# Performance work log

Measured on AMD Instinct MI355X. Metric: run time of the kernel, lower is better.

Reference implementation:

```python
import jax, jax.numpy as jnp
import numpy as np

EMBED_DIM = 1024
NUM_HEADS = 16
HEAD_DIM = EMBED_DIM // NUM_HEADS
EXPANSION = 4
EPS = 1e-5


def setup_inputs() -> dict:
    key = jax.random.key(0)
    ks = jax.random.split(key, 8)
    D, F = EMBED_DIM, EMBED_DIM * EXPANSION
    s = lambda d: 1.0 / np.sqrt(d)
    return {
        "x": jax.random.normal(ks[0], (8, 1024, D), jnp.float32),
        "qkv_w": jax.random.normal(ks[1], (D, 3 * D), jnp.float32) * s(D),
        "qkv_b": jnp.zeros((3 * D,), jnp.float32),
        "out_w": jax.random.normal(ks[2], (D, D), jnp.float32) * s(D),
        "out_b": jnp.zeros((D,), jnp.float32),
        "ffn_w1": jax.random.normal(ks[3], (D, F), jnp.float32) * s(D),
        "ffn_b1": jnp.zeros((F,), jnp.float32),
        "ffn_w2": jax.random.normal(ks[4], (F, D), jnp.float32) * s(F),
        "ffn_b2": jnp.zeros((D,), jnp.float32),
        "ln1_g": jnp.ones((D,), jnp.float32),
        "ln1_b": jnp.zeros((D,), jnp.float32),
        "ln2_g": jnp.ones((D,), jnp.float32),
        "ln2_b": jnp.zeros((D,), jnp.float32),
    }


def _layernorm(x, g, b):
    mu = jnp.mean(x, axis=-1, keepdims=True)
    var = jnp.mean(jnp.square(x - mu), axis=-1, keepdims=True)
    return (x - mu) * jax.lax.rsqrt(var + EPS) * g + b


def reference(x, qkv_w, qkv_b, out_w, out_b, ffn_w1, ffn_b1, ffn_w2, ffn_b2,
              ln1_g, ln1_b, ln2_g, ln2_b):
    B, N, D = x.shape
    H, Hd = NUM_HEADS, HEAD_DIM
    scale = Hd ** -0.5

    residual = x
    h = _layernorm(x, ln1_g, ln1_b)
    qkv = h @ qkv_w + qkv_b                      # [B, N, 3D]
    q, k, v = jnp.split(qkv, 3, axis=-1)
    # [B, N, D] -> [B, H, N, Hd]
    reshape = lambda t: t.reshape(B, N, H, Hd).transpose(0, 2, 1, 3)
    q, k, v = reshape(q), reshape(k), reshape(v)

    attn = jnp.einsum("bhnd,bhmd->bhnm", q, k) * scale
    attn = jax.nn.softmax(attn, axis=-1)
    o = jnp.einsum("bhnm,bhmd->bhnd", attn, v)   # [B, H, N, Hd]
    o = o.transpose(0, 2, 1, 3).reshape(B, N, D)
    o = o @ out_w + out_b
    x = residual + o

    residual = x
    h = _layernorm(x, ln2_g, ln2_b)
    h = jax.nn.gelu(h @ ffn_w1 + ffn_b1, approximate=False) @ ffn_w2 + ffn_b2
    return residual + h
```

## Files before the change

kernel.cpp:

```cpp
#include <hip/hip_runtime.h>
#include <hip/hip_bf16.h>


typedef float f32x4 __attribute__((ext_vector_type(4)));
typedef float f32x16 __attribute__((ext_vector_type(16)));
typedef short bf16x8 __attribute__((ext_vector_type(8)));

#define DEV __device__ __forceinline__

DEV f32x4 mfma16(bf16x8 a, bf16x8 b, f32x4 c) {
    return __builtin_amdgcn_mfma_f32_16x16x32_bf16(a, b, c, 0, 0, 0);
}

DEV f32x16 mfma32(bf16x8 a, bf16x8 b, f32x16 c) {
    return __builtin_amdgcn_mfma_f32_32x32x16_bf16(a, b, c, 0, 0, 0);
}

DEV ushort f2bf(float f) {
    union { float f; unsigned u; } v; v.f = f;
    unsigned r = v.u + 0x7FFFu + ((v.u >> 16) & 1u);
    return (ushort)(r >> 16);
}

DEV unsigned cvtpk(float lo, float hi) {
    unsigned r;
    asm("v_cvt_pk_bf16_f32 %0, %1, %2" : "=v"(r) : "v"(lo), "v"(hi));
    return r;
}

DEV void gload_lds16(const void* g, void* l) {
    __builtin_amdgcn_global_load_lds(
        (const __attribute__((address_space(1))) void*)g,
        (__attribute__((address_space(3))) void*)l, 16, 0, 0);
}

template <int N> DEV void vmwait() {
    asm volatile("s_waitcnt vmcnt(%0)" :: "n"(N) : "memory");
}
DEV void lgkm0() {
    asm volatile("s_waitcnt lgkmcnt(0)" ::: "memory");
}

__global__ __launch_bounds__(256) void transpose_w(
    const float* __restrict__ src, ushort* __restrict__ dst, int K, int N)
{
    __shared__ float tile[32][33];
    const int n0 = blockIdx.x * 32, k0 = blockIdx.y * 32;
    const int tx = threadIdx.x, ty = threadIdx.y;
#pragma unroll
    for (int i = 0; i < 32; i += 8)
        tile[ty + i][tx] = src[(size_t)(k0 + ty + i) * N + n0 + tx];
    __syncthreads();
#pragma unroll
    for (int i = 0; i < 32; i += 8)
        dst[(size_t)(n0 + ty + i) * K + k0 + tx] = f2bf(tile[tx][ty + i]);
}

__global__ __launch_bounds__(256) void transpose_v(
    const ushort* __restrict__ qkvb, ushort* __restrict__ vt)
{
    __shared__ ushort tile[32][33];
    const int b = blockIdx.z >> 4, h = blockIdx.z & 15;
    const int n0 = blockIdx.x * 32, d0 = blockIdx.y * 32;
    const int tx = threadIdx.x, ty = threadIdx.y;
#pragma unroll
    for (int i = 0; i < 32; i += 8)
        tile[ty + i][tx] =
            qkvb[(size_t)(b * 1024 + n0 + ty + i) * 3072 + 2048 + h * 64 + d0 + tx];
    __syncthreads();
#pragma unroll
    for (int i = 0; i < 32; i += 8)
        vt[((size_t)(b * 16 + h) * 64 + d0 + ty + i) * 1024 + n0 + tx] = tile[tx][ty + i];
}

__global__ __launch_bounds__(256) void ln_bf16(
    const float* __restrict__ x, const float* __restrict__ gw,
    const float* __restrict__ bw, ushort* __restrict__ out)
{
    const int row = blockIdx.x;
    const int t = threadIdx.x;
    const float4 v = ((const float4*)(x + (size_t)row * 1024))[t];
    float s  = v.x + v.y + v.z + v.w;
    float s2 = v.x * v.x + v.y * v.y + v.z * v.z + v.w * v.w;
#pragma unroll
    for (int off = 32; off; off >>= 1) {
        s  += __shfl_xor(s, off);
        s2 += __shfl_xor(s2, off);
    }
    __shared__ float red[16];
    const int wave = t >> 6, lane = t & 63;
    if (lane == 0) { red[wave] = s; red[8 + wave] = s2; }
    __syncthreads();
    s  = red[0] + red[1] + red[2] + red[3];
    s2 = red[8] + red[9] + red[10] + red[11];
    const float mean = s * (1.0f / 1024.0f);
    const float var  = s2 * (1.0f / 1024.0f) - mean * mean;
    const float rstd = rsqrtf(var + 1e-5f);
    const float4 gv = ((const float4*)gw)[t];
    const float4 bv = ((const float4*)bw)[t];
    ushort4 o;
    o.x = f2bf((v.x - mean) * rstd * gv.x + bv.x);
    o.y = f2bf((v.y - mean) * rstd * gv.y + bv.y);
    o.z = f2bf((v.z - mean) * rstd * gv.z + bv.z);
    o.w = f2bf((v.w - mean) * rstd * gv.w + bv.w);
    ((ushort4*)out)[(size_t)row * 256 + t] = o;
}

template <int BM, int BN, int WM_, int WN_, int EPI>
__global__ __launch_bounds__(512, 2) void gemm4p(
    const ushort* __restrict__ A, const ushort* __restrict__ BT,
    const float* __restrict__ bias, const float* __restrict__ res,
    void* __restrict__ out, int M, int N, int K)
{
    constexpr int BK = 64;
    constexpr int MR = BM / WM_ / 16;
    constexpr int NR = BN / WN_ / 16;
    constexpr int MH = MR / 2;
    constexpr int CM = MH / 2;
    constexpr int LA = (BM / 2) / 64;
    constexpr int LB = (BN / 2) / 64;
    constexpr int VMN = LA + LB;
    constexpr int ABYTES = BM * BK * 2;
    constexpr int BBYTES = BN * BK * 2;

    extern __shared__ __align__(16) char smem[];
#define ASB(b) (smem + (b) * ABYTES)
#define BSB(b) (smem + 2 * ABYTES + (b) * BBYTES)

    const int tid = threadIdx.x;
    const int wave = tid >> 6, lane = tid & 63;
    const int g = lane >> 4, lr = lane & 15;
    const int wr = wave / WN_, wc = wave % WN_;
    const int akey = (lr & 7) << 4;

    const int gx = gridDim.x;
    const int nwg = gx * gridDim.y;
    int id = blockIdx.y * gx + blockIdx.x;
    id = (id & 7) * (nwg >> 3) + (id >> 3);
    const int m0 = (id / gx) * BM, n0 = (id % gx) * BN;

    const int trow = tid >> 3;
    const int tblk = (tid & 7) ^ (trow & 7);
    const ushort* pA = A  + (size_t)(m0 + trow) * K + tblk * 8;
    const ushort* pB = BT + (size_t)(n0 + trow) * K + tblk * 8;
    const int woff = wave * 1024;

#define STAGE_A(b, h, kt) do { \
    _Pragma("unroll") for (int i = 0; i < LA; ++i) \
        gload_lds16(pA + ((size_t)((h) * (BM / 2) + i * 64)) * K + (size_t)(kt) * 64, \
                    ASB(b) + (h) * (BM / 2) * 128 + i * 8192 + woff); \
} while (0)
#define STAGE_B(b, h, kt) do { \
    _Pragma("unroll") for (int i = 0; i < LB; ++i) \
        gload_lds16(pB + ((size_t)((h) * (BN / 2) + i * 64)) * K + (size_t)(kt) * 64, \
                    BSB(b) + (h) * (BN / 2) * 128 + i * 8192 + woff); \
} while (0)

    bf16x8 af[CM][2], bfr[NR][2];
    f32x4 acc[MR][NR] = {};

#define LOAD_A(b, h, cj) do { \
    const char* rb_ = ASB(b) + ((h) * (BM / 2) + wr * ((BM / 2) / WM_) \
                               + (cj) * CM * 16 + lr) * 128; \
    _Pragma("unroll") for (int cm = 0; cm < CM; ++cm) \
    _Pragma("unroll") for (int kk = 0; kk < 2; ++kk) \
        af[cm][kk] = *(const bf16x8*)(rb_ + cm * 2048 + ((kk * 64 + g * 16) ^ akey)); \
} while (0)
#define LOAD_B(b) do { \
    const char* rb_ = BSB(b) + (wc * (BN / WN_) + lr) * 128; \
    _Pragma("unroll") for (int ni = 0; ni < NR; ++ni) \
    _Pragma("unroll") for (int kk = 0; kk < 2; ++kk) \
        bfr[ni][kk] = *(const bf16x8*)(rb_ + ni * 2048 + ((kk * 64 + g * 16) ^ akey)); \
} while (0)
#define MFMA_PH(h, cj) do { \
    __builtin_amdgcn_s_setprio(1); \
    _Pragma("unroll") for (int cm = 0; cm < CM; ++cm) \
    _Pragma("unroll") for (int ni = 0; ni < NR; ++ni) \
    _Pragma("unroll") for (int kk = 0; kk < 2; ++kk) \
        acc[(h) * MH + (cj) * CM + cm][ni] = \
            mfma16(af[cm][kk], bfr[ni][kk], acc[(h) * MH + (cj) * CM + cm][ni]); \
    __builtin_amdgcn_s_setprio(0); \
} while (0)

    const int NT = K >> 6;

    STAGE_A(0, 0, 0); STAGE_A(0, 1, 0); STAGE_B(0, 0, 0); STAGE_B(0, 1, 0);
    STAGE_B(1, 0, 1);
    STAGE_A(1, 0, 1);
    vmwait<VMN>();
    __builtin_amdgcn_s_barrier();

    for (int kt = 0; kt < NT; ++kt) {
        const int b = kt & 1, nb = b ^ 1;
        LOAD_A(b, 0, 0); LOAD_B(b);
        if (kt + 1 < NT) STAGE_B(nb, 1, kt + 1);
        __builtin_amdgcn_s_barrier(); lgkm0();
        MFMA_PH(0, 0);
        LOAD_A(b, 0, 1);
        if (kt + 1 < NT) STAGE_A(nb, 1, kt + 1);
        __builtin_amdgcn_s_barrier(); lgkm0();
        MFMA_PH(0, 1);
        LOAD_A(b, 1, 0);
        if (kt + 2 < NT) STAGE_B(b, 0, kt + 2);
        __builtin_amdgcn_s_barrier(); lgkm0();
        MFMA_PH(1, 0);
        LOAD_A(b, 1, 1);
        if (kt + 2 < NT) { STAGE_A(b, 0, kt + 2); vmwait<VMN>(); }
        else if (kt + 1 < NT) vmwait<0>();
        __builtin_amdgcn_s_barrier(); lgkm0();
        MFMA_PH(1, 1);
    }

#pragma unroll
    for (int mi = 0; mi < MR; ++mi) {
        const int row0 = m0 + (mi / MH) * (BM / 2) + wr * ((BM / 2) / WM_)
                       + (mi % MH) * 16 + 4 * g;
#pragma unroll
        for (int ni = 0; ni < NR; ++ni) {
            const int col = n0 + wc * (BN / WN_) + ni * 16 + lr;
            const float bv = bias[col];
#pragma unroll
            for (int r = 0; r < 4; ++r) {
                float v = acc[mi][ni][r] + bv;
                const size_t idx = (size_t)(row0 + r) * N + col;
                if constexpr (EPI == 1) {
                    ((float*)out)[idx] = v + res[idx];
                } else if constexpr (EPI == 2) {
                    const float u = 1.595769122f * v + 0.071354816f * v * v * v;
                    const float gs = 1.0f / (1.0f + __expf(-u));
                    ((ushort*)out)[idx] = f2bf(v * gs);
                } else {
                    ((ushort*)out)[idx] = f2bf(v);
                }
            }
        }
    }
#undef STAGE_A
#undef STAGE_B
#undef LOAD_A
#undef LOAD_B
#undef MFMA_PH
#undef ASB
#undef BSB
}

__global__ __launch_bounds__(256) void attn_kernel(
    const ushort* __restrict__ qkv, const ushort* __restrict__ vtb,
    ushort* __restrict__ o)
{
    __shared__ __align__(16) ushort Ks[64 * 64];
    __shared__ __align__(16) ushort Vt[64 * 64];

    const int tid = threadIdx.x;
    const int wave = tid >> 6, lane = tid & 63;
    const int lq = lane & 31;
    const int hi = lane >> 5;
    const int l7 = lane & 7;

    const int hwid = blockIdx.x;
    const int logical = (hwid & 7) * 128 + (hwid >> 3);
    const int bh = logical >> 3, qt = logical & 7;
    const int b = bh >> 4, head = bh & 15;
    const int q0 = qt * 128 + wave * 32;

    const size_t base  = (size_t)b * 1024 * 3072;
    const size_t vbase = (size_t)bh * 64 * 1024;

    union BF8 { bf16x8 v; ushort u[8]; unsigned w[4]; };

    BF8 qf[4];
    {
        const ushort* qrow = qkv + base + (size_t)(q0 + lq) * 3072 + head * 64;
#pragma unroll
        for (int s = 0; s < 4; ++s) {
            *(ushort4*)&qf[s].u[0] = *(const ushort4*)(qrow + 16 * s + 4 * hi);
            *(ushort4*)&qf[s].u[4] = *(const ushort4*)(qrow + 16 * s + 8 + 4 * hi);
        }
    }

    const int sr = tid >> 3, sc = tid & 7;
    const int swz = (sc ^ (sr & 7)) << 3;
    const ushort* kg0 = qkv + base + (size_t)sr * 3072 + 1024 + head * 64 + sc * 8;
    const ushort* kg1 = kg0 + (size_t)32 * 3072;
    const ushort* vg0 = vtb + vbase + (size_t)sr * 1024 + sc * 8;
    const ushort* vg1 = vg0 + (size_t)32 * 1024;
    ushort* ksw0 = Ks + sr * 64 + swz;
    ushort* ksw1 = Ks + (sr + 32) * 64 + swz;
    ushort* vsw0 = Vt + sr * 64 + swz;
    ushort* vsw1 = Vt + (sr + 32) * 64 + swz;

    float l_st = 0.f;
    f32x16 oacc[2] = {};

    constexpr float SCL = 0.18033688011112042f;
    constexpr float MBIAS = 12.0f;

    for (int kt = 0; kt < 16; ++kt) {
        const int n0 = kt * 64;
        __syncthreads();
        *(bf16x8*)ksw0 = *(const bf16x8*)(kg0 + (size_t)n0 * 3072);
        *(bf16x8*)ksw1 = *(const bf16x8*)(kg1 + (size_t)n0 * 3072);
        *(bf16x8*)vsw0 = *(const bf16x8*)(vg0 + n0);
        *(bf16x8*)vsw1 = *(const bf16x8*)(vg1 + n0);
        __syncthreads();

        f32x16 sacc[2];
#pragma unroll
        for (int kb = 0; kb < 2; ++kb) {
            f32x16 a = {};
            const ushort* krow = Ks + (kb * 32 + lq) * 64;
#pragma unroll
            for (int s = 0; s < 4; ++s) {
                BF8 kf;
                *(ushort4*)&kf.u[0] = *(const ushort4*)(krow + (((2 * s)     ^ l7) << 3) + 4 * hi);
                *(ushort4*)&kf.u[4] = *(const ushort4*)(krow + (((2 * s + 1) ^ l7) << 3) + 4 * hi);
                a = mfma32(kf.v, qf[s].v, a);
            }
            sacc[kb] = a;
        }

        float p0 = 0.f, p1 = 0.f, p2 = 0.f, p3 = 0.f;
#pragma unroll
        for (int kb = 0; kb < 2; ++kb)
#pragma unroll
            for (int r = 0; r < 16; ++r) {
                const float pe = exp2f(fmaf(sacc[kb][r], SCL, -MBIAS));
                sacc[kb][r] = pe;
                if ((r & 3) == 0)      p0 += pe;
                else if ((r & 3) == 1) p1 += pe;
                else if ((r & 3) == 2) p2 += pe;
                else                   p3 += pe;
            }
        float psum = (p0 + p1) + (p2 + p3);
        psum += __shfl_xor(psum, 32);
        l_st += psum;

#pragma unroll
        for (int kb = 0; kb < 2; ++kb) {
            BF8 pf[2];
#pragma unroll
            for (int t = 0; t < 2; ++t)
#pragma unroll
                for (int w = 0; w < 4; ++w)
                    pf[t].w[w] = cvtpk(sacc[kb][8 * t + 2 * w], sacc[kb][8 * t + 2 * w + 1]);
#pragma unroll
            for (int nb = 0; nb < 2; ++nb) {
                const ushort* vrow = Vt + (nb * 32 + lq) * 64;
#pragma unroll
                for (int t = 0; t < 2; ++t) {
                    BF8 vf;
                    const int blk = 4 * kb + 2 * t;
                    *(ushort4*)&vf.u[0] = *(const ushort4*)(vrow + ((blk       ^ l7) << 3) + 4 * hi);
                    *(ushort4*)&vf.u[4] = *(const ushort4*)(vrow + (((blk + 1) ^ l7) << 3) + 4 * hi);
                    oacc[nb] = mfma32(vf.v, pf[t].v, oacc[nb]);
                }
            }
        }
    }

    const float inv = 1.0f / l_st;
    ushort* orow = o + (size_t)(b * 1024 + q0 + lq) * 1024 + head * 64;
#pragma unroll
    for (int nb = 0; nb < 2; ++nb)
#pragma unroll
        for (int u = 0; u < 4; ++u) {
            uint2 wv;
            wv.x = cvtpk(oacc[nb][4 * u] * inv,     oacc[nb][4 * u + 1] * inv);
            wv.y = cvtpk(oacc[nb][4 * u + 2] * inv, oacc[nb][4 * u + 3] * inv);
            *(uint2*)(orow + nb * 32 + 8 * u + 4 * hi) = wv;
        }
}

extern "C" void kernel_launch(void* const* d_in, const int* in_sizes, int n_in,
                              void* d_out, int out_size, void* d_ws, size_t ws_size,
                              hipStream_t stream)
{
    const float* x      = (const float*)d_in[0];
    const float* qkv_w  = (const float*)d_in[1];
    const float* qkv_b  = (const float*)d_in[2];
    const float* out_w  = (const float*)d_in[3];
    const float* out_b  = (const float*)d_in[4];
    const float* ffn_w1 = (const float*)d_in[5];
    const float* ffn_b1 = (const float*)d_in[6];
    const float* ffn_w2 = (const float*)d_in[7];
    const float* ffn_b2 = (const float*)d_in[8];
    const float* ln1_g  = (const float*)d_in[9];
    const float* ln1_b  = (const float*)d_in[10];
    const float* ln2_g  = (const float*)d_in[11];
    const float* ln2_b  = (const float*)d_in[12];

    constexpr size_t MB = 1u << 20;
    char* ws = (char*)d_ws;
    ushort* wt_qkv = (ushort*)(ws + 0 * MB);
    ushort* wt_out = (ushort*)(ws + 6 * MB);
    ushort* wt_f1  = (ushort*)(ws + 8 * MB);
    ushort* wt_f2  = (ushort*)(ws + 16 * MB);
    float*  x1     = (float*) (ws + 24 * MB);
    ushort* vtb    = (ushort*)(ws + 24 * MB);
    ushort* hbuf   = (ushort*)(ws + 56 * MB);
    ushort* qkvb   = (ushort*)(ws + 72 * MB);
    ushort* obuf   = (ushort*)(ws + 120 * MB);
    ushort* gbuf   = (ushort*)(ws + 72 * MB);

    const dim3 tb(32, 8);
    transpose_w<<<dim3(3072 / 32, 1024 / 32), tb, 0, stream>>>(qkv_w,  wt_qkv, 1024, 3072);
    transpose_w<<<dim3(1024 / 32, 1024 / 32), tb, 0, stream>>>(out_w,  wt_out, 1024, 1024);
    transpose_w<<<dim3(4096 / 32, 1024 / 32), tb, 0, stream>>>(ffn_w1, wt_f1,  1024, 4096);
    transpose_w<<<dim3(1024 / 32, 4096 / 32), tb, 0, stream>>>(ffn_w2, wt_f2,  4096, 1024);

    ln_bf16<<<8192, 256, 0, stream>>>(x, ln1_g, ln1_b, hbuf);

    constexpr int LDS_256 = (256 + 256) * 64 * 2 * 2;
    constexpr int LDS_128 = (256 + 128) * 64 * 2 * 2;

    gemm4p<256, 256, 2, 4, 0><<<dim3(12, 32), 512, LDS_256, stream>>>(
        hbuf, wt_qkv, qkv_b, nullptr, qkvb, 8192, 3072, 1024);

    transpose_v<<<dim3(32, 2, 128), tb, 0, stream>>>(qkvb, vtb);

    attn_kernel<<<1024, 256, 0, stream>>>(qkvb, vtb, obuf);

    gemm4p<256, 128, 4, 2, 1><<<dim3(8, 32), 512, LDS_128, stream>>>(
        obuf, wt_out, out_b, x, x1, 8192, 1024, 1024);

    ln_bf16<<<8192, 256, 0, stream>>>(x1, ln2_g, ln2_b, hbuf);

    gemm4p<256, 256, 2, 4, 2><<<dim3(16, 32), 512, LDS_256, stream>>>(
        hbuf, wt_f1, ffn_b1, nullptr, gbuf, 8192, 4096, 1024);

    gemm4p<256, 128, 4, 2, 1><<<dim3(8, 32), 512, LDS_128, stream>>>(
        gbuf, wt_f2, ffn_b2, x1, (float*)d_out, 8192, 1024, 4096);
}
```

Measured before the change: 344.9 us.

## Replace templated GEMM with triple-buffered register-prefetch 256x128 GEMM for all projections

Replaces the double-buffered, barrier-per-quarter gemm4p with a fixed 256x128 tile GEMM that uses three LDS buffers. It double-buffers A/B fragments in registers so LDS reads for the next half overlap the current MFMAs. The QKV and FFN1 GEMMs move from 256x256 tiles to 256x128, which doubles their grid size. The aim is to hide global-to-LDS and LDS-to-register latency behind MFMA work, at the cost of more LDS per block (144 KB), possible lower occupancy, and more A-tile re-reads on the wide GEMMs.

```diff
diff --git a/kernel.cpp b/kernel.cpp
--- a/kernel.cpp
+++ b/kernel.cpp
@@ -106,31 +106,22 @@
     ((ushort4*)out)[(size_t)row * 256 + t] = o;
 }
 
-template <int BM, int BN, int WM_, int WN_, int EPI>
-__global__ __launch_bounds__(512, 2) void gemm4p(
+template <int EPI>
+__global__ __launch_bounds__(512, 2) void gemm_ra(
     const ushort* __restrict__ A, const ushort* __restrict__ BT,
     const float* __restrict__ bias, const float* __restrict__ res,
     void* __restrict__ out, int M, int N, int K)
 {
-    constexpr int BK = 64;
-    constexpr int MR = BM / WM_ / 16;
-    constexpr int NR = BN / WN_ / 16;
-    constexpr int MH = MR / 2;
-    constexpr int CM = MH / 2;
-    constexpr int LA = (BM / 2) / 64;
-    constexpr int LB = (BN / 2) / 64;
-    constexpr int VMN = LA + LB;
+    constexpr int BM = 256, BN = 128, BK = 64;
     constexpr int ABYTES = BM * BK * 2;
-    constexpr int BBYTES = BN * BK * 2;
+    constexpr int BUF = ABYTES + BN * BK * 2;
 
     extern __shared__ __align__(16) char smem[];
-#define ASB(b) (smem + (b) * ABYTES)
-#define BSB(b) (smem + 2 * ABYTES + (b) * BBYTES)
 
     const int tid = threadIdx.x;
     const int wave = tid >> 6, lane = tid & 63;
     const int g = lane >> 4, lr = lane & 15;
-    const int wr = wave / WN_, wc = wave % WN_;
+    const int wr = wave >> 1, wc = wave & 1;
     const int akey = (lr & 7) << 4;
 
     const int gx = gridDim.x;
@@ -145,79 +136,89 @@
     const ushort* pB = BT + (size_t)(n0 + trow) * K + tblk * 8;
     const int woff = wave * 1024;
 
-#define STAGE_A(b, h, kt) do { \
-    _Pragma("unroll") for (int i = 0; i < LA; ++i) \
-        gload_lds16(pA + ((size_t)((h) * (BM / 2) + i * 64)) * K + (size_t)(kt) * 64, \
-                    ASB(b) + (h) * (BM / 2) * 128 + i * 8192 + woff); \
+#define STAGE_A(dst, kt) do { \
+    _Pragma("unroll") for (int i = 0; i < 4; ++i) \
+        gload_lds16(pA + (size_t)(i * 64) * K + (size_t)(kt) * 64, \
+                    (dst) + i * 8192 + woff); \
 } while (0)
-#define STAGE_B(b, h, kt) do { \
-    _Pragma("unroll") for (int i = 0; i < LB; ++i) \
-        gload_lds16(pB + ((size_t)((h) * (BN / 2) + i * 64)) * K + (size_t)(kt) * 64, \
-                    BSB(b) + (h) * (BN / 2) * 128 + i * 8192 + woff); \
+#define STAGE_B(dst, kt) do { \
+    _Pragma("unroll") for (int i = 0; i < 2; ++i) \
+        gload_lds16(pB + (size_t)(i * 64) * K + (size_t)(kt) * 64, \
+                    (dst) + ABYTES + i * 8192 + woff); \
 } while (0)
 
-    bf16x8 af[CM][2], bfr[NR][2];
-    f32x4 acc[MR][NR] = {};
-
-#define LOAD_A(b, h, cj) do { \
-    const char* rb_ = ASB(b) + ((h) * (BM / 2) + wr * ((BM / 2) / WM_) \
-                               + (cj) * CM * 16 + lr) * 128; \
-    _Pragma("unroll") for (int cm = 0; cm < CM; ++cm) \
+    bf16x8 aX[2][2], aY[2][2], bP[4][2], bQ[4][2];
+    f32x4 acc[4][4] = {};
+
+#define READ_A(SET, buf, h) do { \
+    const char* rb_ = (buf) + (wr * 64 + (h) * 32 + lr) * 128; \
+    _Pragma("unroll") for (int mi = 0; mi < 2; ++mi) \
     _Pragma("unroll") for (int kk = 0; kk < 2; ++kk) \
-        af[cm][kk] = *(const bf16x8*)(rb_ + cm * 2048 + ((kk * 64 + g * 16) ^ akey)); \
+        SET[mi][kk] = *(const bf16x8*)(rb_ + mi * 2048 + ((kk * 64 + g * 16) ^ akey)); \
 } while (0)
-#define LOAD_B(b) do { \
-    const char* rb_ = BSB(b) + (wc * (BN / WN_) + lr) * 128; \
-    _Pragma("unroll") for (int ni = 0; ni < NR; ++ni) \
+#define READ_B(SET, buf) do { \
+    const char* rb_ = (buf) + ABYTES + (wc * 64 + lr) * 128; \
+    _Pragma("unroll") for (int ni = 0; ni < 4; ++ni) \
     _Pragma("unroll") for (int kk = 0; kk < 2; ++kk) \
-        bfr[ni][kk] = *(const bf16x8*)(rb_ + ni * 2048 + ((kk * 64 + g * 16) ^ akey)); \
+        SET[ni][kk] = *(const bf16x8*)(rb_ + ni * 2048 + ((kk * 64 + g * 16) ^ akey)); \
 } while (0)
-#define MFMA_PH(h, cj) do { \
+#define MFMA_H(ASET, h, BSET) do { \
     __builtin_amdgcn_s_setprio(1); \
-    _Pragma("unroll") for (int cm = 0; cm < CM; ++cm) \
-    _Pragma("unroll") for (int ni = 0; ni < NR; ++ni) \
     _Pragma("unroll") for (int kk = 0; kk < 2; ++kk) \
-        acc[(h) * MH + (cj) * CM + cm][ni] = \
-            mfma16(af[cm][kk], bfr[ni][kk], acc[(h) * MH + (cj) * CM + cm][ni]); \
+    _Pragma("unroll") for (int mi = 0; mi < 2; ++mi) \
+    _Pragma("unroll") for (int ni = 0; ni < 4; ++ni) \
+        acc[(h) * 2 + mi][ni] = \
+            mfma16(ASET[mi][kk], BSET[ni][kk], acc[(h) * 2 + mi][ni]); \
     __builtin_amdgcn_s_setprio(0); \
 } while (0)
+#define BAR() __builtin_amdgcn_s_barrier()
 
     const int NT = K >> 6;
 
-    STAGE_A(0, 0, 0); STAGE_A(0, 1, 0); STAGE_B(0, 0, 0); STAGE_B(0, 1, 0);
-    STAGE_B(1, 0, 1);
-    STAGE_A(1, 0, 1);
-    vmwait<VMN>();
-    __builtin_amdgcn_s_barrier();
-
-    for (int kt = 0; kt < NT; ++kt) {
-        const int b = kt & 1, nb = b ^ 1;
-        LOAD_A(b, 0, 0); LOAD_B(b);
-        if (kt + 1 < NT) STAGE_B(nb, 1, kt + 1);
-        __builtin_amdgcn_s_barrier(); lgkm0();
-        MFMA_PH(0, 0);
-        LOAD_A(b, 0, 1);
-        if (kt + 1 < NT) STAGE_A(nb, 1, kt + 1);
-        __builtin_amdgcn_s_barrier(); lgkm0();
-        MFMA_PH(0, 1);
-        LOAD_A(b, 1, 0);
-        if (kt + 2 < NT) STAGE_B(b, 0, kt + 2);
-        __builtin_amdgcn_s_barrier(); lgkm0();
-        MFMA_PH(1, 0);
-        LOAD_A(b, 1, 1);
-        if (kt + 2 < NT) { STAGE_A(b, 0, kt + 2); vmwait<VMN>(); }
-        else if (kt + 1 < NT) vmwait<0>();
-        __builtin_amdgcn_s_barrier(); lgkm0();
-        MFMA_PH(1, 1);
+    char* pb0 = smem;
+    char* pb1 = smem + BUF;
+    char* pb2 = smem + 2 * BUF;
+
+    STAGE_A(pb0, 0); STAGE_B(pb0, 0);
+    STAGE_A(pb1, 1); STAGE_B(pb1, 1);
+    vmwait<6>();
+    BAR();
+    READ_A(aX, pb0, 0);
+    READ_B(bP, pb0);
+
+    for (int t = 0; t < NT; t += 2) {
+        lgkm0();
+        READ_A(aY, pb0, 1);
+        if (t + 2 < NT) STAGE_A(pb2, t + 2);
+        MFMA_H(aX, 0, bP);
+        if (t + 2 < NT) vmwait<4>(); else vmwait<0>();
+        BAR();
+        lgkm0();
+        READ_A(aX, pb1, 0);
+        READ_B(bQ, pb1);
+        if (t + 2 < NT) STAGE_B(pb2, t + 2);
+        MFMA_H(aY, 1, bP);
+        BAR();
+        lgkm0();
+        READ_A(aY, pb1, 1);
+        if (t + 3 < NT) STAGE_A(pb0, t + 3);
+        MFMA_H(aX, 0, bQ);
+        if (t + 3 < NT) vmwait<4>(); else vmwait<0>();
+        BAR();
+        lgkm0();
+        if (t + 2 < NT) { READ_A(aX, pb2, 0); READ_B(bP, pb2); }
+        if (t + 3 < NT) STAGE_B(pb0, t + 3);
+        MFMA_H(aY, 1, bQ);
+        BAR();
+        char* tmp = pb0; pb0 = pb2; pb2 = pb1; pb1 = tmp;
     }
 
 #pragma unroll
-    for (int mi = 0; mi < MR; ++mi) {
-        const int row0 = m0 + (mi / MH) * (BM / 2) + wr * ((BM / 2) / WM_)
-                       + (mi % MH) * 16 + 4 * g;
-#pragma unroll
-        for (int ni = 0; ni < NR; ++ni) {
-            const int col = n0 + wc * (BN / WN_) + ni * 16 + lr;
+    for (int mi = 0; mi < 4; ++mi) {
+        const int row0 = m0 + wr * 64 + mi * 16 + 4 * g;
+#pragma unroll
+        for (int ni = 0; ni < 4; ++ni) {
+            const int col = n0 + wc * 64 + ni * 16 + lr;
             const float bv = bias[col];
 #pragma unroll
             for (int r = 0; r < 4; ++r) {
@@ -237,11 +238,10 @@
     }
 #undef STAGE_A
 #undef STAGE_B
-#undef LOAD_A
-#undef LOAD_B
-#undef MFMA_PH
-#undef ASB
-#undef BSB
+#undef READ_A
+#undef READ_B
+#undef MFMA_H
+#undef BAR
 }
 
 __global__ __launch_bounds__(256) void attn_kernel(
@@ -410,24 +410,23 @@
 
     ln_bf16<<<8192, 256, 0, stream>>>(x, ln1_g, ln1_b, hbuf);
 
-    constexpr int LDS_256 = (256 + 256) * 64 * 2 * 2;
-    constexpr int LDS_128 = (256 + 128) * 64 * 2 * 2;
-
-    gemm4p<256, 256, 2, 4, 0><<<dim3(12, 32), 512, LDS_256, stream>>>(
+    constexpr int LDS_RA = 3 * (256 * 64 * 2 + 128 * 64 * 2);
+
+    gemm_ra<0><<<dim3(24, 32), 512, LDS_RA, stream>>>(
         hbuf, wt_qkv, qkv_b, nullptr, qkvb, 8192, 3072, 1024);
 
     transpose_v<<<dim3(32, 2, 128), tb, 0, stream>>>(qkvb, vtb);
 
     attn_kernel<<<1024, 256, 0, stream>>>(qkvb, vtb, obuf);
 
-    gemm4p<256, 128, 4, 2, 1><<<dim3(8, 32), 512, LDS_128, stream>>>(
+    gemm_ra<1><<<dim3(8, 32), 512, LDS_RA, stream>>>(
         obuf, wt_out, out_b, x, x1, 8192, 1024, 1024);
 
     ln_bf16<<<8192, 256, 0, stream>>>(x1, ln2_g, ln2_b, hbuf);
 
-    gemm4p<256, 256, 2, 4, 2><<<dim3(16, 32), 512, LDS_256, stream>>>(
+    gemm_ra<2><<<dim3(32, 32), 512, LDS_RA, stream>>>(
         hbuf, wt_f1, ffn_b1, nullptr, gbuf, 8192, 4096, 1024);
 
-    gemm4p<256, 128, 4, 2, 1><<<dim3(8, 32), 512, LDS_128, stream>>>(
+    gemm_ra<1><<<dim3(8, 32), 512, LDS_RA, stream>>>(
         gbuf, wt_f2, ffn_b2, x1, (float*)d_out, 8192, 1024, 4096);
 }
```

Result: slower. 353.4 us (+2.5%).

## Store mid-block residual in bf16, fold attention scale into QKV GEMM, retile QKV

Applied to the files above, without the earlier changes.

The attention-output GEMM now writes the intermediate residual x1 as bf16 instead of fp32. A new bf16-input LayerNorm kernel and a new FFN2 epilogue (EPI 3) read that bf16 residual, which cuts memory traffic on the intermediate. The softmax scale (including log2e) is applied to the Q columns in the QKV GEMM epilogue, and the constant exp bias is removed, so the attention inner loop calls exp2 directly on the scores. The QKV GEMM switches from 256x256 to 256x128 tiles with twice as many blocks. The trade-offs are reduced precision on the residual path and no overflow guard in the softmax exponent.

```diff
diff --git a/kernel.cpp b/kernel.cpp
--- a/kernel.cpp
+++ b/kernel.cpp
@@ -22,6 +22,11 @@
     return (ushort)(r >> 16);
 }
 
+DEV float bf2f(ushort u) {
+    union { unsigned u; float f; } v; v.u = (unsigned)u << 16;
+    return v.f;
+}
+
 DEV unsigned cvtpk(float lo, float hi) {
     unsigned r;
     asm("v_cvt_pk_bf16_f32 %0, %1, %2" : "=v"(r) : "v"(lo), "v"(hi));
@@ -40,6 +45,8 @@
 DEV void lgkm0() {
     asm volatile("s_waitcnt lgkmcnt(0)" ::: "memory");
 }
+
+constexpr float ATT_SCL = 0.18033688011112042f;
 
 __global__ __launch_bounds__(256) void transpose_w(
     const float* __restrict__ src, ushort* __restrict__ dst, int K, int N)
@@ -106,6 +113,40 @@
     ((ushort4*)out)[(size_t)row * 256 + t] = o;
 }
 
+__global__ __launch_bounds__(256) void ln_bf16b(
+    const ushort* __restrict__ x, const float* __restrict__ gw,
+    const float* __restrict__ bw, ushort* __restrict__ out)
+{
+    const int row = blockIdx.x;
+    const int t = threadIdx.x;
+    const ushort4 uv = ((const ushort4*)(x + (size_t)row * 1024))[t];
+    float vx = bf2f(uv.x), vy = bf2f(uv.y), vz = bf2f(uv.z), vw = bf2f(uv.w);
+    float s  = vx + vy + vz + vw;
+    float s2 = vx * vx + vy * vy + vz * vz + vw * vw;
+#pragma unroll
+    for (int off = 32; off; off >>= 1) {
+        s  += __shfl_xor(s, off);
+        s2 += __shfl_xor(s2, off);
+    }
+    __shared__ float red[16];
+    const int wave = t >> 6, lane = t & 63;
+    if (lane == 0) { red[wave] = s; red[8 + wave] = s2; }
+    __syncthreads();
+    s  = red[0] + red[1] + red[2] + red[3];
+    s2 = red[8] + red[9] + red[10] + red[11];
+    const float mean = s * (1.0f / 1024.0f);
+    const float var  = s2 * (1.0f / 1024.0f) - mean * mean;
+    const float rstd = rsqrtf(var + 1e-5f);
+    const float4 gv = ((const float4*)gw)[t];
+    const float4 bv = ((const float4*)bw)[t];
+    ushort4 o;
+    o.x = f2bf((vx - mean) * rstd * gv.x + bv.x);
+    o.y = f2bf((vy - mean) * rstd * gv.y + bv.y);
+    o.z = f2bf((vz - mean) * rstd * gv.z + bv.z);
+    o.w = f2bf((vw - mean) * rstd * gv.w + bv.w);
+    ((ushort4*)out)[(size_t)row * 256 + t] = o;
+}
+
 template <int BM, int BN, int WM_, int WN_, int EPI>
 __global__ __launch_bounds__(512, 2) void gemm4p(
     const ushort* __restrict__ A, const ushort* __restrict__ BT,
@@ -116,7 +157,7 @@
     constexpr int MR = BM / WM_ / 16;
     constexpr int NR = BN / WN_ / 16;
     constexpr int MH = MR / 2;
-    constexpr int CM = MH / 2;
+    constexpr int CM = MH / 2 > 0 ? MH / 2 : 1;
     constexpr int LA = (BM / 2) / 64;
     constexpr int LB = (BN / 2) / 64;
     constexpr int VMN = LA + LB;
@@ -224,12 +265,15 @@
                 float v = acc[mi][ni][r] + bv;
                 const size_t idx = (size_t)(row0 + r) * N + col;
                 if constexpr (EPI == 1) {
-                    ((float*)out)[idx] = v + res[idx];
+                    ((ushort*)out)[idx] = f2bf(v + res[idx]);
                 } else if constexpr (EPI == 2) {
                     const float u = 1.595769122f * v + 0.071354816f * v * v * v;
                     const float gs = 1.0f / (1.0f + __expf(-u));
                     ((ushort*)out)[idx] = f2bf(v * gs);
+                } else if constexpr (EPI == 3) {
+                    ((float*)out)[idx] = v + bf2f(((const ushort*)res)[idx]);
                 } else {
+                    if (col < 1024) v *= ATT_SCL;
                     ((ushort*)out)[idx] = f2bf(v);
                 }
             }
@@ -292,9 +336,6 @@
     float l_st = 0.f;
     f32x16 oacc[2] = {};
 
-    constexpr float SCL = 0.18033688011112042f;
-    constexpr float MBIAS = 12.0f;
-
     for (int kt = 0; kt < 16; ++kt) {
         const int n0 = kt * 64;
         __syncthreads();
@@ -324,7 +365,7 @@
         for (int kb = 0; kb < 2; ++kb)
 #pragma unroll
             for (int r = 0; r < 16; ++r) {
-                const float pe = exp2f(fmaf(sacc[kb][r], SCL, -MBIAS));
+                const float pe = exp2f(sacc[kb][r]);
                 sacc[kb][r] = pe;
                 if ((r & 3) == 0)      p0 += pe;
                 else if ((r & 3) == 1) p1 += pe;
@@ -395,8 +436,8 @@
     ushort* wt_out = (ushort*)(ws + 6 * MB);
     ushort* wt_f1  = (ushort*)(ws + 8 * MB);
     ushort* wt_f2  = (ushort*)(ws + 16 * MB);
-    float*  x1     = (float*) (ws + 24 * MB);
-    ushort* vtb    = (ushort*)(ws + 24 * MB);
+    ushort* x1b    = (ushort*)(ws + 24 * MB);
+    ushort* vtb    = (ushort*)(ws + 40 * MB);
     ushort* hbuf   = (ushort*)(ws + 56 * MB);
     ushort* qkvb   = (ushort*)(ws + 72 * MB);
     ushort* obuf   = (ushort*)(ws + 120 * MB);
@@ -413,7 +454,7 @@
     constexpr int LDS_256 = (256 + 256) * 64 * 2 * 2;
     constexpr int LDS_128 = (256 + 128) * 64 * 2 * 2;
 
-    gemm4p<256, 256, 2, 4, 0><<<dim3(12, 32), 512, LDS_256, stream>>>(
+    gemm4p<256, 128, 4, 2, 4><<<dim3(24, 32), 512, LDS_128, stream>>>(
         hbuf, wt_qkv, qkv_b, nullptr, qkvb, 8192, 3072, 1024);
 
     transpose_v<<<dim3(32, 2, 128), tb, 0, stream>>>(qkvb, vtb);
@@ -421,13 +462,13 @@
     attn_kernel<<<1024, 256, 0, stream>>>(qkvb, vtb, obuf);
 
     gemm4p<256, 128, 4, 2, 1><<<dim3(8, 32), 512, LDS_128, stream>>>(
-        obuf, wt_out, out_b, x, x1, 8192, 1024, 1024);
-
-    ln_bf16<<<8192, 256, 0, stream>>>(x1, ln2_g, ln2_b, hbuf);
+        obuf, wt_out, out_b, x, x1b, 8192, 1024, 1024);
+
+    ln_bf16b<<<8192, 256, 0, stream>>>(x1b, ln2_g, ln2_b, hbuf);
 
     gemm4p<256, 256, 2, 4, 2><<<dim3(16, 32), 512, LDS_256, stream>>>(
         hbuf, wt_f1, ffn_b1, nullptr, gbuf, 8192, 4096, 1024);
 
-    gemm4p<256, 128, 4, 2, 1><<<dim3(8, 32), 512, LDS_128, stream>>>(
-        gbuf, wt_f2, ffn_b2, x1, (float*)d_out, 8192, 1024, 4096);
-}
+    gemm4p<256, 128, 4, 2, 3><<<dim3(8, 32), 512, LDS_128, stream>>>(
+        gbuf, wt_f2, ffn_b2, (const float*)x1b, (float*)d_out, 8192, 1024, 4096);
+}
```

Measured after the change: 335.0 us. 2.9% less time.
